# Performance work log

Measured on AMD Instinct MI355X. Metric: run time of the kernel, lower is better.

Reference implementation:

```python
import jax, jax.numpy as jnp
import numpy as np

N, E, F_IN, HID, EF, C = 100000, 1600000, 64, 64, 32, 4

def setup_inputs() -> dict:
    key = jax.random.key(0)
    ks = jax.random.split(key, 24)
    def p(k, shape, scale=0.05):
        return jax.random.normal(k, shape, dtype=jnp.float32) * scale
    return dict(
        x=jax.random.normal(ks[0], (N, F_IN), dtype=jnp.float32),
        edge_index=jax.random.randint(ks[1], (2, E), 0, N, dtype=jnp.int32),
        edge_attr=jax.random.normal(ks[2], (E, EF), dtype=jnp.float32),
        # GCNConv weights for update (z), reset (r), candidate (h) gates
        Wz=p(ks[3], (F_IN, HID)), bz=jnp.zeros((HID,), jnp.float32),
        Wr=p(ks[4], (F_IN, HID)), br=jnp.zeros((HID,), jnp.float32),
        Wh=p(ks[5], (F_IN, HID)), bh=jnp.zeros((HID,), jnp.float32),
        # gate linear layers: Linear(2*HID, HID)
        Wlz=p(ks[6], (2 * HID, HID)), blz=jnp.zeros((HID,), jnp.float32),
        Wlr=p(ks[7], (2 * HID, HID)), blr=jnp.zeros((HID,), jnp.float32),
        Wlh=p(ks[8], (2 * HID, HID)), blh=jnp.zeros((HID,), jnp.float32),
        # edge predictor MLP: Linear(2*HID+EF, HID) -> ReLU -> Dropout(eval) -> Linear(HID, C)
        W1=p(ks[9], (2 * HID + EF, HID)), b1=jnp.zeros((HID,), jnp.float32),
        W2=p(ks[10], (HID, C)), b2=jnp.zeros((C,), jnp.float32),
    )

def _gcn(x, W, b, src, dst, norm, n):
    # GCNConv: out = D^-1/2 (A+I) D^-1/2 (x @ W) + b; src/dst already include self-loops
    xw = x @ W  # [N, HID]
    agg = jax.ops.segment_sum(xw[src] * norm[:, None], dst, num_segments=n)
    return agg + b

def reference(x, edge_index, edge_attr, Wz, bz, Wr, br, Wh, bh,
              Wlz, blz, Wlr, blr, Wlh, blh, W1, b1, W2, b2):
    n = x.shape[0]
    src, dst = edge_index[0], edge_index[1]
    # add self-loops for GCN normalization
    loop = jnp.arange(n, dtype=src.dtype)
    s = jnp.concatenate([src, loop])
    d = jnp.concatenate([dst, loop])
    deg = jax.ops.segment_sum(jnp.ones(s.shape[0], dtype=x.dtype), d, num_segments=n)
    dinv = jax.lax.rsqrt(jnp.maximum(deg, 1.0))
    norm = dinv[s] * dinv[d]  # symmetric normalization per edge
    # TGCN cell, initial hidden state H = zeros
    H0 = jnp.zeros((n, Wz.shape[1]), dtype=x.dtype)
    Z = jax.nn.sigmoid(jnp.concatenate([_gcn(x, Wz, bz, s, d, norm, n), H0], axis=1) @ Wlz + blz)
    R = jax.nn.sigmoid(jnp.concatenate([_gcn(x, Wr, br, s, d, norm, n), H0], axis=1) @ Wlr + blr)
    Ht = jnp.tanh(jnp.concatenate([_gcn(x, Wh, bh, s, d, norm, n), H0 * R], axis=1) @ Wlh + blh)
    h = Z * H0 + (1.0 - Z) * Ht  # [N, HID]
    # edge predictor on original edges (no self-loops)
    emb = jnp.concatenate([h[src], h[dst], edge_attr], axis=1)  # [E, 2*HID+EF]
    hid = jax.nn.relu(emb @ W1 + b1)  # Dropout(0.5) is identity in eval mode
    return hid @ W2 + b2  # [E, C]
```

## Files before the change

kernel.cpp:

```cpp
#include <hip/hip_runtime.h>

#define F 64
#define EF 32
#define COUT 4

typedef unsigned int uint;
typedef unsigned short ushort;
typedef __attribute__((ext_vector_type(8))) short bf16x8;
typedef __attribute__((ext_vector_type(4))) float f32x4;

__device__ inline ushort f2bf(float f) {
    uint u = __float_as_uint(f);
    return (ushort)((u + 0x7fff + ((u >> 16) & 1)) >> 16);
}
__device__ inline float bf2f(ushort u) {
    return __uint_as_float(((uint)u) << 16);
}


__global__ void k_deg(const int* __restrict__ dst, int* __restrict__ deg, int E) {
    int i = blockIdx.x * blockDim.x + threadIdx.x;
    if (i < E) atomicAdd(&deg[dst[i]], 1);
}

__global__ void k_dinv(const int* __restrict__ deg, float* __restrict__ dinv, int n) {
    int i = blockIdx.x * blockDim.x + threadIdx.x;
    if (i < n) dinv[i] = rsqrtf((float)(deg[i] + 1));
}

__global__ void k_xcast(const float* __restrict__ x, ushort* __restrict__ xb, int n4) {
    int i = blockIdx.x * 256 + threadIdx.x;
    if (i >= n4) return;
    float4 v = *(const float4*)(x + (size_t)i * 4);
    ushort4 o;
    o.x = f2bf(v.x); o.y = f2bf(v.y); o.z = f2bf(v.z); o.w = f2bf(v.w);
    *(ushort4*)(xb + (size_t)i * 4) = o;
}


__global__ void k_blocksum(const int* __restrict__ deg, int* __restrict__ bsum, int n) {
    __shared__ int sm[256];
    int i = blockIdx.x * 256 + threadIdx.x;
    sm[threadIdx.x] = (i < n) ? deg[i] : 0;
    __syncthreads();
    for (int s = 128; s > 0; s >>= 1) {
        if (threadIdx.x < s) sm[threadIdx.x] += sm[threadIdx.x + s];
        __syncthreads();
    }
    if (threadIdx.x == 0) bsum[blockIdx.x] = sm[0];
}

__global__ void k_scanb(const int* __restrict__ bsum, int* __restrict__ boffs, int nb) {
    int lane = threadIdx.x;
    int carry = 0;
    for (int base = 0; base < nb; base += 64) {
        int v = (base + lane < nb) ? bsum[base + lane] : 0;
        int incl = v;
        #pragma unroll
        for (int off = 1; off < 64; off <<= 1) {
            int t = __shfl_up(incl, off);
            if (lane >= off) incl += t;
        }
        if (base + lane < nb) boffs[base + lane] = carry + incl - v;
        carry += __shfl(incl, 63);
    }
}

__global__ void k_rowptr(const int* __restrict__ deg, const int* __restrict__ boffs,
                         int* __restrict__ rowptr, int n) {
    __shared__ int sm[256];
    int tid = threadIdx.x;
    int i = blockIdx.x * 256 + tid;
    int v = (i < n) ? deg[i] : 0;
    sm[tid] = v;
    __syncthreads();
    for (int off = 1; off < 256; off <<= 1) {
        int t = (tid >= off) ? sm[tid - off] : 0;
        __syncthreads();
        sm[tid] += t;
        __syncthreads();
    }
    if (i < n) rowptr[i] = boffs[blockIdx.x] + sm[tid] - v;
}

__global__ void k_bucket(const int* __restrict__ src, const int* __restrict__ dst,
                         const int* __restrict__ rowptr, int* __restrict__ fill,
                         int* __restrict__ es, int E) {
    int e = blockIdx.x * 256 + threadIdx.x;
    if (e >= E) return;
    int d = dst[e];
    int pos = rowptr[d] + atomicAdd(&fill[d], 1);
    es[pos] = src[e];
}

__global__ __launch_bounds__(256) void k_agg(
    const ushort* __restrict__ xb, const float* __restrict__ dinv,
    const int* __restrict__ es, const int* __restrict__ rowptr,
    const int* __restrict__ deg, ushort* __restrict__ xaggb, int n) {
    int node = (blockIdx.x * 256 + threadIdx.x) >> 6;
    int lane = threadIdx.x & 63;
    if (node >= n) return;
    int lg = lane >> 4, lc = lane & 15;
    int start = rowptr[node], cnt = deg[node];
    float di = dinv[node];
    float a0 = 0.f, a1 = 0.f, a2 = 0.f, a3 = 0.f;
    for (int base = 0; base < cnt; base += 4) {
        int k = base + lg;
        float w = 0.f;
        size_t off = 0;
        if (k < cnt) {
            int s = es[start + k];
            w = dinv[s] * di;
            off = (size_t)s * F;
        }
        uint2 r = make_uint2(0u, 0u);
        if (k < cnt) r = *(const uint2*)(xb + off + lc * 4);
        a0 += w * __uint_as_float(r.x << 16);
        a1 += w * __uint_as_float(r.x & 0xffff0000u);
        a2 += w * __uint_as_float(r.y << 16);
        a3 += w * __uint_as_float(r.y & 0xffff0000u);
    }
    a0 += __shfl_xor(a0, 16); a0 += __shfl_xor(a0, 32);
    a1 += __shfl_xor(a1, 16); a1 += __shfl_xor(a1, 32);
    a2 += __shfl_xor(a2, 16); a2 += __shfl_xor(a2, 32);
    a3 += __shfl_xor(a3, 16); a3 += __shfl_xor(a3, 32);
    if (lg == 0) {
        float dd = di * di;
        uint2 xv = *(const uint2*)(xb + (size_t)node * F + lc * 4);
        a0 += dd * __uint_as_float(xv.x << 16);
        a1 += dd * __uint_as_float(xv.x & 0xffff0000u);
        a2 += dd * __uint_as_float(xv.y << 16);
        a3 += dd * __uint_as_float(xv.y & 0xffff0000u);
        ushort4 o;
        o.x = f2bf(a0); o.y = f2bf(a1); o.z = f2bf(a2); o.w = f2bf(a3);
        *(ushort4*)(xaggb + (size_t)node * F + lc * 4) = o;
    }
}

__global__ void k_weights(const float* __restrict__ Wz, const float* __restrict__ bz,
                          const float* __restrict__ Wh, const float* __restrict__ bh,
                          const float* __restrict__ Wlz, const float* __restrict__ blz,
                          const float* __restrict__ Wlh, const float* __restrict__ blh,
                          ushort* __restrict__ B1t, float* __restrict__ V) {
    int j = threadIdx.x;
    int k = blockIdx.x;
    if (k < 64) {
        float sz = 0.f, sh = 0.f;
        for (int i = 0; i < 64; ++i) {
            sz += Wz[k * 64 + i] * Wlz[i * 64 + j];
            sh += Wh[k * 64 + i] * Wlh[i * 64 + j];
        }
        B1t[j * 64 + k]        = f2bf(sz);
        B1t[(64 + j) * 64 + k] = f2bf(sh);
    } else {
        float sz = blz[j], sh = blh[j];
        for (int i = 0; i < 64; ++i) {
            sz += bz[i] * Wlz[i * 64 + j];
            sh += bh[i] * Wlh[i * 64 + j];
        }
        V[j]      = sz;
        V[64 + j] = sh;
    }
}

__global__ void k_wcast(const float* __restrict__ W1, ushort* __restrict__ B2t,
                        ushort* __restrict__ W1cTb) {
    int i = blockIdx.x * 256 + threadIdx.x;
    if (i < 8192) {
        int c = i >> 6, k = i & 63;
        int row = (c < 64) ? k : (64 + k);
        B2t[i] = f2bf(W1[row * 64 + (c & 63)]);
    }
    int t = i - 8192;
    if (t >= 0 && t < 2048) {
        int j = t >> 5, k = t & 31;
        W1cTb[t] = f2bf(W1[(128 + k) * 64 + j]);
    }
}

__global__ __launch_bounds__(256) void k_node(
    const ushort* __restrict__ xaggb, const ushort* __restrict__ B1t,
    const ushort* __restrict__ B2t, const float* __restrict__ V,
    const float* __restrict__ b1,
    ushort* __restrict__ Pb, ushort* __restrict__ Qb, int n) {
    __shared__ ushort hsm[64 * 64];
    int wid = threadIdx.x >> 6, lane = threadIdx.x & 63;
    int lg = lane >> 4, lc = lane & 15;
    int base = blockIdx.x * 64;

    bf16x8 b1f[2][2], b2f[2][2];
    #pragma unroll
    for (int t = 0; t < 2; ++t) {
        int c1 = ((t ? wid + 4 : wid) * 16 + lc) * 64;
        int c2 = ((wid * 2 + t) * 16 + lc) * 64;
        #pragma unroll
        for (int ks = 0; ks < 2; ++ks) {
            b1f[t][ks] = *(const bf16x8*)(B1t + c1 + ks * 32 + lg * 8);
            b2f[t][ks] = *(const bf16x8*)(B2t + c2 + ks * 32 + lg * 8);
        }
    }
    float vzc = V[wid * 16 + lc], vhc = V[64 + wid * 16 + lc];
    float bP[2];
    #pragma unroll
    for (int t = 0; t < 2; ++t) {
        int c2 = (wid * 2 + t) * 16 + lc;
        bP[t] = (c2 < 64) ? b1[c2] : 0.f;
    }

    const f32x4 fz = {0.f, 0.f, 0.f, 0.f};
    f32x4 accZ[4], accT[4];
    #pragma unroll
    for (int rt = 0; rt < 4; ++rt) { accZ[rt] = fz; accT[rt] = fz; }

    #pragma unroll
    for (int rt = 0; rt < 4; ++rt) {
        const ushort* ap = xaggb + (size_t)(base + rt * 16 + lc) * 64 + lg * 8;
        bf16x8 a0 = *(const bf16x8*)(ap);
        bf16x8 a1 = *(const bf16x8*)(ap + 32);
        accZ[rt] = __builtin_amdgcn_mfma_f32_16x16x32_bf16(a0, b1f[0][0], accZ[rt], 0, 0, 0);
        accZ[rt] = __builtin_amdgcn_mfma_f32_16x16x32_bf16(a1, b1f[0][1], accZ[rt], 0, 0, 0);
        accT[rt] = __builtin_amdgcn_mfma_f32_16x16x32_bf16(a0, b1f[1][0], accT[rt], 0, 0, 0);
        accT[rt] = __builtin_amdgcn_mfma_f32_16x16x32_bf16(a1, b1f[1][1], accT[rt], 0, 0, 0);
    }

    #pragma unroll
    for (int rt = 0; rt < 4; ++rt) {
        #pragma unroll
        for (int r = 0; r < 4; ++r) {
            float z = 1.f / (1.f + __expf(-(accZ[rt][r] + vzc)));
            float tt = tanhf(accT[rt][r] + vhc);
            float h = (1.f - z) * tt;
            int row = rt * 16 + lg * 4 + r;
            int byte = ((row * 64 + wid * 16 + lc) * 2) ^ ((row & 7) << 4);
            *(ushort*)((char*)hsm + byte) = f2bf(h);
        }
    }
    __syncthreads();

    f32x4 acc2[2][4];
    #pragma unroll
    for (int rt = 0; rt < 4; ++rt) { acc2[0][rt] = fz; acc2[1][rt] = fz; }
    #pragma unroll
    for (int rt = 0; rt < 4; ++rt) {
        #pragma unroll
        for (int ks = 0; ks < 2; ++ks) {
            int row = rt * 16 + lc;
            int byte = (row * 128 + ks * 64 + lg * 16) ^ ((row & 7) << 4);
            bf16x8 a2 = *(const bf16x8*)((char*)hsm + byte);
            acc2[0][rt] = __builtin_amdgcn_mfma_f32_16x16x32_bf16(a2, b2f[0][ks], acc2[0][rt], 0, 0, 0);
            acc2[1][rt] = __builtin_amdgcn_mfma_f32_16x16x32_bf16(a2, b2f[1][ks], acc2[1][rt], 0, 0, 0);
        }
    }

    ushort* dstb = (wid < 2) ? Pb : Qb;
    #pragma unroll
    for (int t = 0; t < 2; ++t) {
        int cl = ((wid * 2 + t) * 16 + lc) & 63;
        #pragma unroll
        for (int rt = 0; rt < 4; ++rt) {
            #pragma unroll
            for (int r = 0; r < 4; ++r) {
                int node = base + rt * 16 + lg * 4 + r;
                if (node < n) dstb[(size_t)node * 64 + cl] = f2bf(acc2[t][rt][r] + bP[t]);
            }
        }
    }
}

__global__ __launch_bounds__(256) void k_edge2(
    const int* __restrict__ src, const int* __restrict__ dst,
    const float* __restrict__ attr,
    const ushort* __restrict__ Pb, const ushort* __restrict__ Qb,
    const ushort* __restrict__ W1cTb,
    const float* __restrict__ W2, const float* __restrict__ b2,
    float* __restrict__ out, int E) {
    __shared__ float w2s[256];
    __shared__ float b2s[4];
    w2s[threadIdx.x] = W2[threadIdx.x];
    if (threadIdx.x < 4) b2s[threadIdx.x] = b2[threadIdx.x];
    __syncthreads();

    int wid = threadIdx.x >> 6, lane = threadIdx.x & 63;
    int lg = lane >> 4, lc = lane & 15;
    int we = (blockIdx.x * 4 + wid) * 64;
    if (we >= E) return;

    int idx = we + lane; if (idx >= E) idx = E - 1;
    int sR = src[idx], dR = dst[idx];

    bf16x8 aW[4];
    #pragma unroll
    for (int rt = 0; rt < 4; ++rt)
        aW[rt] = *(const bf16x8*)(W1cTb + (rt * 16 + lc) * 32 + lg * 8);

    const f32x4 fz = {0.f, 0.f, 0.f, 0.f};
    #pragma unroll
    for (int et = 0; et < 4; ++et) {
        int erow = et * 16 + lc;
        int eid_e = we + erow; if (eid_e >= E) eid_e = E - 1;
        int s_e = __shfl(sR, erow);
        int d_e = __shfl(dR, erow);

        const float* ap = attr + (size_t)eid_e * EF + lg * 8;
        float4 a0 = *(const float4*)(ap);
        float4 a1 = *(const float4*)(ap + 4);
        bf16x8 bfr;
        bfr[0] = (short)f2bf(a0.x); bfr[1] = (short)f2bf(a0.y);
        bfr[2] = (short)f2bf(a0.z); bfr[3] = (short)f2bf(a0.w);
        bfr[4] = (short)f2bf(a1.x); bfr[5] = (short)f2bf(a1.y);
        bfr[6] = (short)f2bf(a1.z); bfr[7] = (short)f2bf(a1.w);

        f32x4 acc[4];
        #pragma unroll
        for (int rt = 0; rt < 4; ++rt) acc[rt] = fz;
        #pragma unroll
        for (int rt = 0; rt < 4; ++rt)
            acc[rt] = __builtin_amdgcn_mfma_f32_16x16x32_bf16(aW[rt], bfr, acc[rt], 0, 0, 0);

        const ushort* Ps = Pb + (size_t)s_e * F;
        const ushort* Qd = Qb + (size_t)d_e * F;
        float o0 = 0.f, o1 = 0.f, o2 = 0.f, o3 = 0.f;
        #pragma unroll
        for (int rt = 0; rt < 4; ++rt) {
            int j0 = rt * 16 + lg * 4;
            uint2 pv = *(const uint2*)(Ps + j0);
            uint2 qv = *(const uint2*)(Qd + j0);
            float p0 = __uint_as_float(pv.x << 16), p1 = __uint_as_float(pv.x & 0xffff0000u);
            float p2 = __uint_as_float(pv.y << 16), p3 = __uint_as_float(pv.y & 0xffff0000u);
            float q0 = __uint_as_float(qv.x << 16), q1 = __uint_as_float(qv.x & 0xffff0000u);
            float q2 = __uint_as_float(qv.y << 16), q3 = __uint_as_float(qv.y & 0xffff0000u);
            float h0 = fmaxf(acc[rt][0] + p0 + q0, 0.f);
            float h1 = fmaxf(acc[rt][1] + p1 + q1, 0.f);
            float h2 = fmaxf(acc[rt][2] + p2 + q2, 0.f);
            float h3 = fmaxf(acc[rt][3] + p3 + q3, 0.f);
            float4 w0 = *(const float4*)(&w2s[(j0 + 0) * 4]);
            float4 w1 = *(const float4*)(&w2s[(j0 + 1) * 4]);
            float4 w2v = *(const float4*)(&w2s[(j0 + 2) * 4]);
            float4 w3 = *(const float4*)(&w2s[(j0 + 3) * 4]);
            o0 += h0 * w0.x + h1 * w1.x + h2 * w2v.x + h3 * w3.x;
            o1 += h0 * w0.y + h1 * w1.y + h2 * w2v.y + h3 * w3.y;
            o2 += h0 * w0.z + h1 * w1.z + h2 * w2v.z + h3 * w3.z;
            o3 += h0 * w0.w + h1 * w1.w + h2 * w2v.w + h3 * w3.w;
        }
        o0 += __shfl_xor(o0, 16); o0 += __shfl_xor(o0, 32);
        o1 += __shfl_xor(o1, 16); o1 += __shfl_xor(o1, 32);
        o2 += __shfl_xor(o2, 16); o2 += __shfl_xor(o2, 32);
        o3 += __shfl_xor(o3, 16); o3 += __shfl_xor(o3, 32);
        if (lg == 0 && (we + erow) < E)
            *(float4*)(out + (size_t)(we + erow) * 4) =
                make_float4(o0 + b2s[0], o1 + b2s[1], o2 + b2s[2], o3 + b2s[3]);
    }
}


extern "C" void kernel_launch(void* const* d_in, const int* in_sizes, int n_in,
                              void* d_out, int out_size, void* d_ws, size_t ws_size,
                              hipStream_t stream) {
    const float* x    = (const float*)d_in[0];
    const int*   ei   = (const int*)d_in[1];
    const float* attr = (const float*)d_in[2];
    const float* Wz   = (const float*)d_in[3];
    const float* bz   = (const float*)d_in[4];
    const float* Wh   = (const float*)d_in[7];
    const float* bh   = (const float*)d_in[8];
    const float* Wlz  = (const float*)d_in[9];
    const float* blz  = (const float*)d_in[10];
    const float* Wlh  = (const float*)d_in[13];
    const float* blh  = (const float*)d_in[14];
    const float* W1   = (const float*)d_in[15];
    const float* b1   = (const float*)d_in[16];
    const float* W2   = (const float*)d_in[17];
    const float* b2   = (const float*)d_in[18];
    float* out = (float*)d_out;

    const int N = in_sizes[0] / F;
    const int E = in_sizes[1] / 2;
    const int* src = ei;
    const int* dst = ei + E;
    const int NB = (N + 255) / 256;
    const int NBT = (N + 63) / 64;

    ushort* xaggb = (ushort*)d_ws;
    ushort* regB  = xaggb + (size_t)N * F;
    ushort* Qb    = regB + (size_t)N * F;
    ushort* B1t   = Qb + (size_t)N * F;
    ushort* B2t   = B1t + 8192;
    ushort* W1cTb = B2t + 8192;
    float*  V     = (float*)(W1cTb + 2048);
    int*    es    = (int*)(V + 128);
    int*    deg   = es + E;
    float*  dinv  = (float*)(deg + N);
    int*    rowptr= (int*)(dinv + N);
    int*    fill  = rowptr + N;
    int*    bsum  = fill + N;
    int*    boffs = bsum + 512;
    ushort* xb = regB;
    ushort* Pb = regB;

    hipMemsetAsync(deg, 0, (size_t)N * sizeof(int), stream);
    hipMemsetAsync(fill, 0, (size_t)N * sizeof(int), stream);

    k_deg<<<(E + 255) / 256, 256, 0, stream>>>(dst, deg, E);
    k_dinv<<<NB, 256, 0, stream>>>(deg, dinv, N);
    k_weights<<<65, 64, 0, stream>>>(Wz, bz, Wh, bh, Wlz, blz, Wlh, blh, B1t, V);
    k_wcast<<<40, 256, 0, stream>>>(W1, B2t, W1cTb);
    k_xcast<<<(N * F / 4 + 255) / 256, 256, 0, stream>>>(x, xb, N * F / 4);

    k_blocksum<<<NB, 256, 0, stream>>>(deg, bsum, N);
    k_scanb<<<1, 64, 0, stream>>>(bsum, boffs, NB);
    k_rowptr<<<NB, 256, 0, stream>>>(deg, boffs, rowptr, N);
    k_bucket<<<(E + 255) / 256, 256, 0, stream>>>(src, dst, rowptr, fill, es, E);

    k_agg<<<(N * 64 + 255) / 256, 256, 0, stream>>>(xb, dinv, es, rowptr, deg, xaggb, N);

    k_node<<<NBT, 256, 0, stream>>>(xaggb, B1t, B2t, V, b1, Pb, Qb, N);

    k_edge2<<<(E + 255) / 256, 256, 0, stream>>>(src, dst, attr, Pb, Qb, W1cTb, W2, b2, out, E);
}
```

Measured before the change: 428.0 us.

## Pack dinv with source index, unroll agg gathers, prefetch edge gathers

The bucketing kernel now stores each edge's source index together with its precomputed dinv[src] as an int2, so the aggregation kernel no longer makes a dependent random dinv lookup per edge. The aggregation loop handles two edges per lane group per iteration to raise the number of gathers in flight. The edge kernel issues all attribute and P/Q row loads for its four edge tiles before the MFMA and compute loop, so memory latency overlaps. In exchange the bucket array doubles in size and the edge kernel needs more registers, which may lower occupancy.

```diff
diff --git a/kernel.cpp b/kernel.cpp
--- a/kernel.cpp
+++ b/kernel.cpp
@@ -84,18 +84,19 @@
 }
 
 __global__ void k_bucket(const int* __restrict__ src, const int* __restrict__ dst,
+                         const float* __restrict__ dinv,
                          const int* __restrict__ rowptr, int* __restrict__ fill,
-                         int* __restrict__ es, int E) {
+                         int2* __restrict__ es2, int E) {
     int e = blockIdx.x * 256 + threadIdx.x;
     if (e >= E) return;
-    int d = dst[e];
+    int d = dst[e], s = src[e];
     int pos = rowptr[d] + atomicAdd(&fill[d], 1);
-    es[pos] = src[e];
+    es2[pos] = make_int2(s, __float_as_int(dinv[s]));
 }
 
 __global__ __launch_bounds__(256) void k_agg(
     const ushort* __restrict__ xb, const float* __restrict__ dinv,
-    const int* __restrict__ es, const int* __restrict__ rowptr,
+    const int2* __restrict__ es2, const int* __restrict__ rowptr,
     const int* __restrict__ deg, ushort* __restrict__ xaggb, int n) {
     int node = (blockIdx.x * 256 + threadIdx.x) >> 6;
     int lane = threadIdx.x & 63;
@@ -104,21 +105,21 @@
     int start = rowptr[node], cnt = deg[node];
     float di = dinv[node];
     float a0 = 0.f, a1 = 0.f, a2 = 0.f, a3 = 0.f;
-    for (int base = 0; base < cnt; base += 4) {
-        int k = base + lg;
-        float w = 0.f;
-        size_t off = 0;
-        if (k < cnt) {
-            int s = es[start + k];
-            w = dinv[s] * di;
-            off = (size_t)s * F;
-        }
-        uint2 r = make_uint2(0u, 0u);
-        if (k < cnt) r = *(const uint2*)(xb + off + lc * 4);
-        a0 += w * __uint_as_float(r.x << 16);
-        a1 += w * __uint_as_float(r.x & 0xffff0000u);
-        a2 += w * __uint_as_float(r.y << 16);
-        a3 += w * __uint_as_float(r.y & 0xffff0000u);
+    for (int base = 0; base < cnt; base += 8) {
+        int k0 = base + lg, k1 = base + lg + 4;
+        bool v0 = k0 < cnt, v1 = k1 < cnt;
+        int2 e0 = make_int2(0, 0), e1 = make_int2(0, 0);
+        if (v0) e0 = es2[start + k0];
+        if (v1) e1 = es2[start + k1];
+        uint2 r0 = make_uint2(0u, 0u), r1 = make_uint2(0u, 0u);
+        if (v0) r0 = *(const uint2*)(xb + (size_t)e0.x * F + lc * 4);
+        if (v1) r1 = *(const uint2*)(xb + (size_t)e1.x * F + lc * 4);
+        float w0 = v0 ? __int_as_float(e0.y) * di : 0.f;
+        float w1 = v1 ? __int_as_float(e1.y) * di : 0.f;
+        a0 += w0 * __uint_as_float(r0.x << 16)         + w1 * __uint_as_float(r1.x << 16);
+        a1 += w0 * __uint_as_float(r0.x & 0xffff0000u) + w1 * __uint_as_float(r1.x & 0xffff0000u);
+        a2 += w0 * __uint_as_float(r0.y << 16)         + w1 * __uint_as_float(r1.y << 16);
+        a3 += w0 * __uint_as_float(r0.y & 0xffff0000u) + w1 * __uint_as_float(r1.y & 0xffff0000u);
     }
     a0 += __shfl_xor(a0, 16); a0 += __shfl_xor(a0, 32);
     a1 += __shfl_xor(a1, 16); a1 += __shfl_xor(a1, 32);
@@ -293,22 +294,44 @@
     for (int rt = 0; rt < 4; ++rt)
         aW[rt] = *(const bf16x8*)(W1cTb + (rt * 16 + lc) * 32 + lg * 8);
 
-    const f32x4 fz = {0.f, 0.f, 0.f, 0.f};
+    int s_e[4], d_e[4], eid_e[4];
     #pragma unroll
     for (int et = 0; et < 4; ++et) {
         int erow = et * 16 + lc;
-        int eid_e = we + erow; if (eid_e >= E) eid_e = E - 1;
-        int s_e = __shfl(sR, erow);
-        int d_e = __shfl(dR, erow);
-
-        const float* ap = attr + (size_t)eid_e * EF + lg * 8;
-        float4 a0 = *(const float4*)(ap);
-        float4 a1 = *(const float4*)(ap + 4);
+        int e = we + erow; if (e >= E) e = E - 1;
+        eid_e[et] = e;
+        s_e[et] = __shfl(sR, erow);
+        d_e[et] = __shfl(dR, erow);
+    }
+
+    float4 at0[4], at1[4];
+    #pragma unroll
+    for (int et = 0; et < 4; ++et) {
+        const float* ap = attr + (size_t)eid_e[et] * EF + lg * 8;
+        at0[et] = *(const float4*)(ap);
+        at1[et] = *(const float4*)(ap + 4);
+    }
+    uint2 pv[4][4], qv[4][4];
+    #pragma unroll
+    for (int et = 0; et < 4; ++et) {
+        const ushort* Ps = Pb + (size_t)s_e[et] * F;
+        const ushort* Qd = Qb + (size_t)d_e[et] * F;
+        #pragma unroll
+        for (int rt = 0; rt < 4; ++rt) {
+            int j0 = rt * 16 + lg * 4;
+            pv[et][rt] = *(const uint2*)(Ps + j0);
+            qv[et][rt] = *(const uint2*)(Qd + j0);
+        }
+    }
+
+    const f32x4 fz = {0.f, 0.f, 0.f, 0.f};
+    #pragma unroll
+    for (int et = 0; et < 4; ++et) {
         bf16x8 bfr;
-        bfr[0] = (short)f2bf(a0.x); bfr[1] = (short)f2bf(a0.y);
-        bfr[2] = (short)f2bf(a0.z); bfr[3] = (short)f2bf(a0.w);
-        bfr[4] = (short)f2bf(a1.x); bfr[5] = (short)f2bf(a1.y);
-        bfr[6] = (short)f2bf(a1.z); bfr[7] = (short)f2bf(a1.w);
+        bfr[0] = (short)f2bf(at0[et].x); bfr[1] = (short)f2bf(at0[et].y);
+        bfr[2] = (short)f2bf(at0[et].z); bfr[3] = (short)f2bf(at0[et].w);
+        bfr[4] = (short)f2bf(at1[et].x); bfr[5] = (short)f2bf(at1[et].y);
+        bfr[6] = (short)f2bf(at1[et].z); bfr[7] = (short)f2bf(at1[et].w);
 
         f32x4 acc[4];
         #pragma unroll
@@ -317,18 +340,15 @@
         for (int rt = 0; rt < 4; ++rt)
             acc[rt] = __builtin_amdgcn_mfma_f32_16x16x32_bf16(aW[rt], bfr, acc[rt], 0, 0, 0);
 
-        const ushort* Ps = Pb + (size_t)s_e * F;
-        const ushort* Qd = Qb + (size_t)d_e * F;
         float o0 = 0.f, o1 = 0.f, o2 = 0.f, o3 = 0.f;
         #pragma unroll
         for (int rt = 0; rt < 4; ++rt) {
             int j0 = rt * 16 + lg * 4;
-            uint2 pv = *(const uint2*)(Ps + j0);
-            uint2 qv = *(const uint2*)(Qd + j0);
-            float p0 = __uint_as_float(pv.x << 16), p1 = __uint_as_float(pv.x & 0xffff0000u);
-            float p2 = __uint_as_float(pv.y << 16), p3 = __uint_as_float(pv.y & 0xffff0000u);
-            float q0 = __uint_as_float(qv.x << 16), q1 = __uint_as_float(qv.x & 0xffff0000u);
-            float q2 = __uint_as_float(qv.y << 16), q3 = __uint_as_float(qv.y & 0xffff0000u);
+            uint2 p = pv[et][rt], q = qv[et][rt];
+            float p0 = __uint_as_float(p.x << 16), p1 = __uint_as_float(p.x & 0xffff0000u);
+            float p2 = __uint_as_float(p.y << 16), p3 = __uint_as_float(p.y & 0xffff0000u);
+            float q0 = __uint_as_float(q.x << 16), q1 = __uint_as_float(q.x & 0xffff0000u);
+            float q2 = __uint_as_float(q.y << 16), q3 = __uint_as_float(q.y & 0xffff0000u);
             float h0 = fmaxf(acc[rt][0] + p0 + q0, 0.f);
             float h1 = fmaxf(acc[rt][1] + p1 + q1, 0.f);
             float h2 = fmaxf(acc[rt][2] + p2 + q2, 0.f);
@@ -346,6 +366,7 @@
         o1 += __shfl_xor(o1, 16); o1 += __shfl_xor(o1, 32);
         o2 += __shfl_xor(o2, 16); o2 += __shfl_xor(o2, 32);
         o3 += __shfl_xor(o3, 16); o3 += __shfl_xor(o3, 32);
+        int erow = et * 16 + lc;
         if (lg == 0 && (we + erow) < E)
             *(float4*)(out + (size_t)(we + erow) * 4) =
                 make_float4(o0 + b2s[0], o1 + b2s[1], o2 + b2s[2], o3 + b2s[3]);
@@ -387,8 +408,8 @@
     ushort* B2t   = B1t + 8192;
     ushort* W1cTb = B2t + 8192;
     float*  V     = (float*)(W1cTb + 2048);
-    int*    es    = (int*)(V + 128);
-    int*    deg   = es + E;
+    int2*   es2   = (int2*)(V + 128);
+    int*    deg   = (int*)(es2 + (size_t)E);
     float*  dinv  = (float*)(deg + N);
     int*    rowptr= (int*)(dinv + N);
     int*    fill  = rowptr + N;
@@ -409,9 +430,9 @@
     k_blocksum<<<NB, 256, 0, stream>>>(deg, bsum, N);
     k_scanb<<<1, 64, 0, stream>>>(bsum, boffs, NB);
     k_rowptr<<<NB, 256, 0, stream>>>(deg, boffs, rowptr, N);
-    k_bucket<<<(E + 255) / 256, 256, 0, stream>>>(src, dst, rowptr, fill, es, E);
-
-    k_agg<<<(N * 64 + 255) / 256, 256, 0, stream>>>(xb, dinv, es, rowptr, deg, xaggb, N);
+    k_bucket<<<(E + 255) / 256, 256, 0, stream>>>(src, dst, dinv, rowptr, fill, es2, E);
+
+    k_agg<<<(N * 64 + 255) / 256, 256, 0, stream>>>(xb, dinv, es2, rowptr, deg, xaggb, N);
 
     k_node<<<NBT, 256, 0, stream>>>(xaggb, B1t, B2t, V, b1, Pb, Qb, N);
 
```

Result: faster. 401.1 us (-6.3%).

## Store packed CSR edge records and process edges in destination-sorted order

Applied to the files above, without the earlier changes.

The bucket kernel now writes a packed int4 record per edge (src, dinv[src], original edge id, dst) in CSR order. The aggregation kernel reads dinv from that record, so the separate gather is gone, and it processes 16 neighbors per iteration using 16-byte row loads. The edge-predictor kernel walks edges in destination-sorted order and scatters outputs by original edge id, which improves locality of the Q (dst) gathers. In exchange, reads of edge_attr and the output writes become scattered, and the edge-list workspace grows fourfold.

```diff
diff --git a/kernel.cpp b/kernel.cpp
--- a/kernel.cpp
+++ b/kernel.cpp
@@ -16,6 +16,8 @@
 __device__ inline float bf2f(ushort u) {
     return __uint_as_float(((uint)u) << 16);
 }
+__device__ inline float blo(uint u) { return __uint_as_float(u << 16); }
+__device__ inline float bhi(uint u) { return __uint_as_float(u & 0xffff0000u); }
 
 
 __global__ void k_deg(const int* __restrict__ dst, int* __restrict__ deg, int E) {
@@ -84,56 +86,68 @@
 }
 
 __global__ void k_bucket(const int* __restrict__ src, const int* __restrict__ dst,
+                         const float* __restrict__ dinv,
                          const int* __restrict__ rowptr, int* __restrict__ fill,
-                         int* __restrict__ es, int E) {
+                         int4* __restrict__ es4, int E) {
     int e = blockIdx.x * 256 + threadIdx.x;
     if (e >= E) return;
-    int d = dst[e];
+    int d = dst[e], s = src[e];
     int pos = rowptr[d] + atomicAdd(&fill[d], 1);
-    es[pos] = src[e];
+    es4[pos] = make_int4(s, __float_as_int(dinv[s]), e, d);
 }
 
 __global__ __launch_bounds__(256) void k_agg(
     const ushort* __restrict__ xb, const float* __restrict__ dinv,
-    const int* __restrict__ es, const int* __restrict__ rowptr,
+    const int4* __restrict__ es4, const int* __restrict__ rowptr,
     const int* __restrict__ deg, ushort* __restrict__ xaggb, int n) {
     int node = (blockIdx.x * 256 + threadIdx.x) >> 6;
     int lane = threadIdx.x & 63;
     if (node >= n) return;
-    int lg = lane >> 4, lc = lane & 15;
+    int slot = lane >> 3, oct = lane & 7;
     int start = rowptr[node], cnt = deg[node];
     float di = dinv[node];
-    float a0 = 0.f, a1 = 0.f, a2 = 0.f, a3 = 0.f;
-    for (int base = 0; base < cnt; base += 4) {
-        int k = base + lg;
-        float w = 0.f;
-        size_t off = 0;
-        if (k < cnt) {
-            int s = es[start + k];
-            w = dinv[s] * di;
-            off = (size_t)s * F;
-        }
-        uint2 r = make_uint2(0u, 0u);
-        if (k < cnt) r = *(const uint2*)(xb + off + lc * 4);
-        a0 += w * __uint_as_float(r.x << 16);
-        a1 += w * __uint_as_float(r.x & 0xffff0000u);
-        a2 += w * __uint_as_float(r.y << 16);
-        a3 += w * __uint_as_float(r.y & 0xffff0000u);
-    }
-    a0 += __shfl_xor(a0, 16); a0 += __shfl_xor(a0, 32);
-    a1 += __shfl_xor(a1, 16); a1 += __shfl_xor(a1, 32);
-    a2 += __shfl_xor(a2, 16); a2 += __shfl_xor(a2, 32);
-    a3 += __shfl_xor(a3, 16); a3 += __shfl_xor(a3, 32);
-    if (lg == 0) {
+    float a0 = 0.f, a1 = 0.f, a2 = 0.f, a3 = 0.f, a4 = 0.f, a5 = 0.f, a6 = 0.f, a7 = 0.f;
+    for (int base = 0; base < cnt; base += 16) {
+        int k0 = base + slot, k1 = base + slot + 8;
+        bool v0 = k0 < cnt, v1 = k1 < cnt;
+        int4 e0 = make_int4(0, 0, 0, 0), e1 = make_int4(0, 0, 0, 0);
+        if (v0) e0 = es4[start + k0];
+        if (v1) e1 = es4[start + k1];
+        uint4 r0 = make_uint4(0u, 0u, 0u, 0u), r1 = make_uint4(0u, 0u, 0u, 0u);
+        if (v0) r0 = *(const uint4*)(xb + (size_t)e0.x * F + oct * 8);
+        if (v1) r1 = *(const uint4*)(xb + (size_t)e1.x * F + oct * 8);
+        float w0 = v0 ? __int_as_float(e0.y) * di : 0.f;
+        float w1 = v1 ? __int_as_float(e1.y) * di : 0.f;
+        a0 += w0 * blo(r0.x) + w1 * blo(r1.x);
+        a1 += w0 * bhi(r0.x) + w1 * bhi(r1.x);
+        a2 += w0 * blo(r0.y) + w1 * blo(r1.y);
+        a3 += w0 * bhi(r0.y) + w1 * bhi(r1.y);
+        a4 += w0 * blo(r0.z) + w1 * blo(r1.z);
+        a5 += w0 * bhi(r0.z) + w1 * bhi(r1.z);
+        a6 += w0 * blo(r0.w) + w1 * blo(r1.w);
+        a7 += w0 * bhi(r0.w) + w1 * bhi(r1.w);
+    }
+    a0 += __shfl_xor(a0, 8); a0 += __shfl_xor(a0, 16); a0 += __shfl_xor(a0, 32);
+    a1 += __shfl_xor(a1, 8); a1 += __shfl_xor(a1, 16); a1 += __shfl_xor(a1, 32);
+    a2 += __shfl_xor(a2, 8); a2 += __shfl_xor(a2, 16); a2 += __shfl_xor(a2, 32);
+    a3 += __shfl_xor(a3, 8); a3 += __shfl_xor(a3, 16); a3 += __shfl_xor(a3, 32);
+    a4 += __shfl_xor(a4, 8); a4 += __shfl_xor(a4, 16); a4 += __shfl_xor(a4, 32);
+    a5 += __shfl_xor(a5, 8); a5 += __shfl_xor(a5, 16); a5 += __shfl_xor(a5, 32);
+    a6 += __shfl_xor(a6, 8); a6 += __shfl_xor(a6, 16); a6 += __shfl_xor(a6, 32);
+    a7 += __shfl_xor(a7, 8); a7 += __shfl_xor(a7, 16); a7 += __shfl_xor(a7, 32);
+    if (slot == 0) {
         float dd = di * di;
-        uint2 xv = *(const uint2*)(xb + (size_t)node * F + lc * 4);
-        a0 += dd * __uint_as_float(xv.x << 16);
-        a1 += dd * __uint_as_float(xv.x & 0xffff0000u);
-        a2 += dd * __uint_as_float(xv.y << 16);
-        a3 += dd * __uint_as_float(xv.y & 0xffff0000u);
-        ushort4 o;
-        o.x = f2bf(a0); o.y = f2bf(a1); o.z = f2bf(a2); o.w = f2bf(a3);
-        *(ushort4*)(xaggb + (size_t)node * F + lc * 4) = o;
+        uint4 xv = *(const uint4*)(xb + (size_t)node * F + oct * 8);
+        a0 += dd * blo(xv.x); a1 += dd * bhi(xv.x);
+        a2 += dd * blo(xv.y); a3 += dd * bhi(xv.y);
+        a4 += dd * blo(xv.z); a5 += dd * bhi(xv.z);
+        a6 += dd * blo(xv.w); a7 += dd * bhi(xv.w);
+        uint4 o;
+        o.x = (uint)f2bf(a0) | ((uint)f2bf(a1) << 16);
+        o.y = (uint)f2bf(a2) | ((uint)f2bf(a3) << 16);
+        o.z = (uint)f2bf(a4) | ((uint)f2bf(a5) << 16);
+        o.w = (uint)f2bf(a6) | ((uint)f2bf(a7) << 16);
+        *(uint4*)(xaggb + (size_t)node * F + oct * 8) = o;
     }
 }
 
@@ -268,7 +282,7 @@
 }
 
 __global__ __launch_bounds__(256) void k_edge2(
-    const int* __restrict__ src, const int* __restrict__ dst,
+    const int4* __restrict__ es4,
     const float* __restrict__ attr,
     const ushort* __restrict__ Pb, const ushort* __restrict__ Qb,
     const ushort* __restrict__ W1cTb,
@@ -286,7 +300,8 @@
     if (we >= E) return;
 
     int idx = we + lane; if (idx >= E) idx = E - 1;
-    int sR = src[idx], dR = dst[idx];
+    int4 e4 = es4[idx];
+    int sR = e4.x, eidR = e4.z, dR = e4.w;
 
     bf16x8 aW[4];
     #pragma unroll
@@ -297,9 +312,9 @@
     #pragma unroll
     for (int et = 0; et < 4; ++et) {
         int erow = et * 16 + lc;
-        int eid_e = we + erow; if (eid_e >= E) eid_e = E - 1;
-        int s_e = __shfl(sR, erow);
-        int d_e = __shfl(dR, erow);
+        int eid_e = __shfl(eidR, erow);
+        int s_e   = __shfl(sR, erow);
+        int d_e   = __shfl(dR, erow);
 
         const float* ap = attr + (size_t)eid_e * EF + lg * 8;
         float4 a0 = *(const float4*)(ap);
@@ -325,10 +340,8 @@
             int j0 = rt * 16 + lg * 4;
             uint2 pv = *(const uint2*)(Ps + j0);
             uint2 qv = *(const uint2*)(Qd + j0);
-            float p0 = __uint_as_float(pv.x << 16), p1 = __uint_as_float(pv.x & 0xffff0000u);
-            float p2 = __uint_as_float(pv.y << 16), p3 = __uint_as_float(pv.y & 0xffff0000u);
-            float q0 = __uint_as_float(qv.x << 16), q1 = __uint_as_float(qv.x & 0xffff0000u);
-            float q2 = __uint_as_float(qv.y << 16), q3 = __uint_as_float(qv.y & 0xffff0000u);
+            float p0 = blo(pv.x), p1 = bhi(pv.x), p2 = blo(pv.y), p3 = bhi(pv.y);
+            float q0 = blo(qv.x), q1 = bhi(qv.x), q2 = blo(qv.y), q3 = bhi(qv.y);
             float h0 = fmaxf(acc[rt][0] + p0 + q0, 0.f);
             float h1 = fmaxf(acc[rt][1] + p1 + q1, 0.f);
             float h2 = fmaxf(acc[rt][2] + p2 + q2, 0.f);
@@ -347,7 +360,7 @@
         o2 += __shfl_xor(o2, 16); o2 += __shfl_xor(o2, 32);
         o3 += __shfl_xor(o3, 16); o3 += __shfl_xor(o3, 32);
         if (lg == 0 && (we + erow) < E)
-            *(float4*)(out + (size_t)(we + erow) * 4) =
+            *(float4*)(out + (size_t)eid_e * 4) =
                 make_float4(o0 + b2s[0], o1 + b2s[1], o2 + b2s[2], o3 + b2s[3]);
     }
 }
@@ -387,8 +400,8 @@
     ushort* B2t   = B1t + 8192;
     ushort* W1cTb = B2t + 8192;
     float*  V     = (float*)(W1cTb + 2048);
-    int*    es    = (int*)(V + 128);
-    int*    deg   = es + E;
+    int4*   es4   = (int4*)(V + 128);
+    int*    deg   = (int*)(es4 + (size_t)E);
     float*  dinv  = (float*)(deg + N);
     int*    rowptr= (int*)(dinv + N);
     int*    fill  = rowptr + N;
@@ -409,11 +422,11 @@
     k_blocksum<<<NB, 256, 0, stream>>>(deg, bsum, N);
     k_scanb<<<1, 64, 0, stream>>>(bsum, boffs, NB);
     k_rowptr<<<NB, 256, 0, stream>>>(deg, boffs, rowptr, N);
-    k_bucket<<<(E + 255) / 256, 256, 0, stream>>>(src, dst, rowptr, fill, es, E);
-
-    k_agg<<<(N * 64 + 255) / 256, 256, 0, stream>>>(xb, dinv, es, rowptr, deg, xaggb, N);
+    k_bucket<<<(E + 255) / 256, 256, 0, stream>>>(src, dst, dinv, rowptr, fill, es4, E);
+
+    k_agg<<<(N * 64 + 255) / 256, 256, 0, stream>>>(xb, dinv, es4, rowptr, deg, xaggb, N);
 
     k_node<<<NBT, 256, 0, stream>>>(xaggb, B1t, B2t, V, b1, Pb, Qb, N);
 
-    k_edge2<<<(E + 255) / 256, 256, 0, stream>>>(src, dst, attr, Pb, Qb, W1cTb, W2, b2, out, E);
-}
+    k_edge2<<<(E + 255) / 256, 256, 0, stream>>>(es4, attr, Pb, Qb, W1cTb, W2, b2, out, E);
+}
```

After: 383.4 us. 10.4% less time.
